# Kernel optimization log

Hardware: AMD Instinct MI355X
Metric: run time of the kernel (lower is better)

Reference implementation:

```python
import jax, jax.numpy as jnp
import numpy as np

WS = 4      # window_size (RSUT5 default)
SHIFT = 2   # window_size // 2
NH = 8      # num_heads
DIM = 256
H0 = W0 = T0 = 32
B0 = 1


def _ln(x, g, b, eps=1e-5):
    m = x.mean(-1, keepdims=True)
    v = ((x - m) ** 2).mean(-1, keepdims=True)
    return (x - m) / jnp.sqrt(v + eps) * g + b


def _rel_index(ws):
    c = np.stack(np.meshgrid(np.arange(ws), np.arange(ws), np.arange(ws), indexing='ij')).reshape(3, -1)
    r = (c[:, :, None] - c[:, None, :]).transpose(1, 2, 0) + (ws - 1)
    return jnp.asarray((r[..., 0] * (2 * ws - 1) + r[..., 1]) * (2 * ws - 1) + r[..., 2])


def _partition(x, ws):
    B, H, W, T, C = x.shape
    x = x.reshape(B, H // ws, ws, W // ws, ws, T // ws, ws, C)
    return x.transpose(0, 1, 3, 5, 2, 4, 6, 7).reshape(-1, ws ** 3, C)


def _reverse(w, ws, B, H, W, T):
    C = w.shape[-1]
    x = w.reshape(B, H // ws, W // ws, T // ws, ws, ws, ws, C)
    return x.transpose(0, 1, 4, 2, 5, 3, 6, 7).reshape(B, H, W, T, C)


def _attn_mask(H, W, T, ws, ss):
    # static (numpy) replica of Block.createmask; H,W,T divisible by ws here
    img = np.zeros((H, W, T), np.float32)
    sls = (slice(0, -ws), slice(-ws, -ss), slice(-ss, None))
    cnt = 0
    for h in sls:
        for w in sls:
            for t in sls:
                img[h, w, t] = cnt
                cnt += 1
    mw = img.reshape(H // ws, ws, W // ws, ws, T // ws, ws).transpose(0, 2, 4, 1, 3, 5).reshape(-1, ws ** 3)
    d = mw[:, None, :] - mw[:, :, None]
    return jnp.asarray(np.where(d != 0, -100.0, 0.0).astype(np.float32))


def _swin(x, H, W, T, shift, mask, n1g, n1b, qkvw, qkvb, rpb, projw, projb, n2g, n2b, fc1w, fc1b, fc2w, fc2b):
    B, L, C = x.shape
    N = WS ** 3
    hd = C // NH
    shortcut = x
    x = _ln(x, n1g, n1b).reshape(B, H, W, T, C)
    if shift:
        x = jnp.roll(x, (-shift, -shift, -shift), axis=(1, 2, 3))
    xw = _partition(x, WS)                                        # [B*nW, N, C]
    qkv = (xw @ qkvw.T + qkvb).reshape(-1, N, 3, NH, hd).transpose(2, 0, 3, 1, 4)
    q, k, v = qkv[0], qkv[1], qkv[2]                              # [B*nW, NH, N, hd]
    attn = jnp.einsum('bhnd,bhmd->bhnm', q * (hd ** -0.5), k)
    attn = attn + rpb[_rel_index(WS)].transpose(2, 0, 1)[None]    # relative position bias
    if mask is not None:
        nW = mask.shape[0]
        attn = (attn.reshape(B, nW, NH, N, N) + mask[None, :, None]).reshape(-1, NH, N, N)
    attn = jax.nn.softmax(attn, axis=-1)
    out = jnp.einsum('bhnm,bhmd->bhnd', attn, v).transpose(0, 2, 1, 3).reshape(-1, N, C)
    out = out @ projw.T + projb
    x = _reverse(out, WS, B, H, W, T)
    if shift:
        x = jnp.roll(x, (shift, shift, shift), axis=(1, 2, 3))
    x = shortcut + x.reshape(B, L, C)
    h = _ln(x, n2g, n2b)
    h = jax.nn.gelu(h @ fc1w.T + fc1b, approximate=False) @ fc2w.T + fc2b
    return x + h


def setup_inputs() -> dict:
    key = jax.random.key(0)
    ks = iter(jax.random.split(key, 16))
    def rn(shape, s=0.02):
        return jax.random.normal(next(ks), shape, jnp.float32) * s
    d = {'x': jax.random.normal(next(ks), (B0, H0 * W0 * T0, DIM), jnp.float32),
         'H': H0, 'W': W0, 'T': T0,
         'norm_g': jnp.ones((DIM,), jnp.float32), 'norm_b': jnp.zeros((DIM,), jnp.float32)}
    for p in ('w', 's'):
        d[p + 'n1g'] = jnp.ones((DIM,), jnp.float32); d[p + 'n1b'] = jnp.zeros((DIM,), jnp.float32)
        d[p + 'qkvw'] = rn((3 * DIM, DIM)); d[p + 'qkvb'] = jnp.zeros((3 * DIM,), jnp.float32)
        d[p + 'rpb'] = rn(((2 * WS - 1) ** 3, NH))
        d[p + 'projw'] = rn((DIM, DIM)); d[p + 'projb'] = jnp.zeros((DIM,), jnp.float32)
        d[p + 'n2g'] = jnp.ones((DIM,), jnp.float32); d[p + 'n2b'] = jnp.zeros((DIM,), jnp.float32)
        d[p + 'fc1w'] = rn((4 * DIM, DIM)); d[p + 'fc1b'] = jnp.zeros((4 * DIM,), jnp.float32)
        d[p + 'fc2w'] = rn((DIM, 4 * DIM)); d[p + 'fc2b'] = jnp.zeros((DIM,), jnp.float32)
    return d


def reference(x, H, W, T, norm_g, norm_b,
              wn1g, wn1b, wqkvw, wqkvb, wrpb, wprojw, wprojb, wn2g, wn2b, wfc1w, wfc1b, wfc2w, wfc2b,
              sn1g, sn1b, sqkvw, sqkvb, srpb, sprojw, sprojb, sn2g, sn2b, sfc1w, sfc1b, sfc2w, sfc2b):
    mask = _attn_mask(H, W, T, WS, SHIFT)
    x = _swin(x, H, W, T, 0, None, wn1g, wn1b, wqkvw, wqkvb, wrpb, wprojw, wprojb, wn2g, wn2b, wfc1w, wfc1b, wfc2w, wfc2b)
    x = _swin(x, H, W, T, SHIFT, mask, sn1g, sn1b, sqkvw, sqkvb, srpb, sprojw, sprojb, sn2g, sn2b, sfc1w, sfc1b, sfc2w, sfc2b)
    B, L, C = x.shape
    # Block.norm + toConv: [B, L, C] -> [B, C, H, W, T]
    return _ln(x, norm_g, norm_b).reshape(B, H, W, T, C).transpose(0, 4, 1, 2, 3)
```

## Files before the change

kernel.cpp:

```cpp
#include <hip/hip_runtime.h>

typedef unsigned short u16;
typedef unsigned int   u32;
typedef __bf16 bfx8 __attribute__((ext_vector_type(8)));
typedef float  fx4  __attribute__((ext_vector_type(4)));

__device__ __forceinline__ u16 f2b(float f) {
    union { float f; u32 i; } v; v.f = f;
    u32 r = (v.i + 0x7fffu + ((v.i >> 16) & 1u)) >> 16;
    return (u16)r;
}
__device__ __forceinline__ u32 pk(float a, float b) {
    return (u32)f2b(a) | ((u32)f2b(b) << 16);
}

__device__ __forceinline__ void gl2lds16(const u16* g, u16* l) {
    __builtin_amdgcn_global_load_lds(
        (const __attribute__((address_space(1))) u32*)(const void*)g,
        (__attribute__((address_space(3))) u32*)(void*)l, 16, 0, 0);
}

__device__ __forceinline__ int map_token(int r, int shift) {
    int win = r >> 6, n = r & 63;
    int wh = win >> 6, ww = (win >> 3) & 7, wt = win & 7;
    int h = wh * 4 + (n >> 4);
    int w = ww * 4 + ((n >> 2) & 3);
    int t = wt * 4 + (n & 3);
    h = (h + shift) & 31; w = (w + shift) & 31; t = (t + shift) & 31;
    return (h << 10) | (w << 5) | t;
}

__device__ __forceinline__ float gelu_fast(float v) {
    float t = v * v;
    float u = v * __builtin_fmaf(t, 0.044715f, 1.0f);
    float e = __expf(-1.5957691216057308f * u);
    return v * __builtin_amdgcn_rcpf(1.0f + e);
}

struct CvtArgs { const float* src[8]; int cum[9]; };
__global__ __launch_bounds__(256) void cvt_kernel(CvtArgs a, u16* __restrict__ dst) {
    int g = (blockIdx.x * 256 + threadIdx.x) * 4;
    int t = 0;
    #pragma unroll
    for (int i = 1; i < 8; i++) t += (g >= a.cum[i]);
    int local = g - a.cum[t];
    float4 f = *(const float4*)(a.src[t] + local);
    uint2 o; o.x = pk(f.x, f.y); o.y = pk(f.z, f.w);
    *(uint2*)(dst + g) = o;
}

template<int GATHER, int F32OUT>
__global__ __launch_bounds__(256) void ln_kernel(const float* __restrict__ resid,
                                                 const float* __restrict__ g, const float* __restrict__ b,
                                                 void* __restrict__ outp, int shift) {
    int lane = threadIdx.x & 63;
    int row  = blockIdx.x * 4 + (threadIdx.x >> 6);
    int src  = GATHER ? map_token(row, shift) : row;
    float4 x = ((const float4*)(resid + src * 256))[lane];
    float s1 = x.x + x.y + x.z + x.w;
    float s2 = x.x * x.x + x.y * x.y + x.z * x.z + x.w * x.w;
    #pragma unroll
    for (int off = 1; off < 64; off <<= 1) { s1 += __shfl_xor(s1, off); s2 += __shfl_xor(s2, off); }
    float mean = s1 * (1.0f / 256.0f);
    float var  = s2 * (1.0f / 256.0f) - mean * mean;
    float rstd = rsqrtf(var + 1e-5f);
    int c = lane * 4;
    float4 gv = *(const float4*)(g + c);
    float4 bv = *(const float4*)(b + c);
    float y0 = (x.x - mean) * rstd * gv.x + bv.x;
    float y1 = (x.y - mean) * rstd * gv.y + bv.y;
    float y2 = (x.z - mean) * rstd * gv.z + bv.z;
    float y3 = (x.w - mean) * rstd * gv.w + bv.w;
    if (F32OUT) {
        float4 o; o.x = y0; o.y = y1; o.z = y2; o.w = y3;
        *(float4*)((float*)outp + row * 256 + c) = o;
    } else {
        uint2 o; o.x = pk(y0, y1); o.y = pk(y2, y3);
        *(uint2*)((u16*)outp + row * 256 + c) = o;
    }
}

template<int EPI>
__global__ __launch_bounds__(256) void gemm2(const u16* __restrict__ A, const u16* __restrict__ W,
                                             const float* __restrict__ bias,
                                             u16* __restrict__ outb, float* __restrict__ resid,
                                             int Nout, int K, int shift,
                                             const float* __restrict__ rsrc) {
    __shared__ u16 As[3][4096];
    __shared__ u16 Bs[3][4096];
    int lane = threadIdx.x & 63, w = threadIdx.x >> 6;
    int wm = w >> 1, wn = w & 1;
    int m0 = blockIdx.x * 128, n0 = blockIdx.y * 128;
    int lr = lane & 15, q = lane >> 4;
    int sw = q ^ ((lr >> 1) & 3);

    int rowS  = w * 16 + (lane >> 2);
    int kg    = (lane & 3) ^ ((rowS >> 1) & 3);
    int slot0 = (w * 64 + lane) * 8;
    int slot1 = slot0 + 2048;
    const u16* gA0 = A + (size_t)(m0 + rowS) * K + kg * 8;
    const u16* gA1 = A + (size_t)(m0 + rowS + 64) * K + kg * 8;
    const u16* gB0 = W + (size_t)(n0 + rowS) * K + kg * 8;
    const u16* gB1 = W + (size_t)(n0 + rowS + 64) * K + kg * 8;

    int oA[4], oB[4];
    #pragma unroll
    for (int t = 0; t < 4; t++) {
        oA[t] = ((wm * 64 + t * 16 + lr) * 4 + sw) * 8;
        oB[t] = ((wn * 64 + t * 16 + lr) * 4 + sw) * 8;
    }

    fx4 acc[4][4] = {};

    auto stage = [&](int kt, int b) {
        gl2lds16(gA0 + kt, &As[b][slot0]);
        gl2lds16(gA1 + kt, &As[b][slot1]);
        gl2lds16(gB0 + kt, &Bs[b][slot0]);
        gl2lds16(gB1 + kt, &Bs[b][slot1]);
    };

    int nk = K >> 5;
    stage(0, 0);
    if (nk > 1) stage(32, 1);
    int b0 = 0, b1 = 1, b2 = 2;
    for (int ki = 0; ki < nk; ki++) {
        if (ki + 1 < nk) asm volatile("s_waitcnt vmcnt(4)" ::: "memory");
        else             asm volatile("s_waitcnt vmcnt(0)" ::: "memory");
        __builtin_amdgcn_s_barrier();
        __builtin_amdgcn_sched_barrier(0);
        if (ki + 2 < nk) stage((ki + 2) << 5, b2);
        bfx8 af[4], bfr[4];
        #pragma unroll
        for (int t = 0; t < 4; t++) {
            af[t]  = *(const bfx8*)(&As[b0][oA[t]]);
            bfr[t] = *(const bfx8*)(&Bs[b0][oB[t]]);
        }
        #pragma unroll
        for (int i = 0; i < 4; i++)
            #pragma unroll
            for (int j = 0; j < 4; j++)
                acc[i][j] = __builtin_amdgcn_mfma_f32_16x16x32_bf16(af[i], bfr[j], acc[i][j], 0, 0, 0);
        int tmp = b0; b0 = b1; b1 = b2; b2 = tmp;
    }

    float bv[4];
    #pragma unroll
    for (int j = 0; j < 4; j++) bv[j] = bias[n0 + wn * 64 + j * 16 + lr];
    #pragma unroll
    for (int i = 0; i < 4; i++) {
        #pragma unroll
        for (int r = 0; r < 4; r++) {
            int gr = m0 + wm * 64 + i * 16 + q * 4 + r;
            int orow = (EPI == 3) ? map_token(gr, shift) : gr;
            #pragma unroll
            for (int j = 0; j < 4; j++) {
                int gc = n0 + wn * 64 + j * 16 + lr;
                float v = acc[i][j][r] + bv[j];
                if (EPI == 0) {
                    outb[(size_t)gr * Nout + gc] = f2b(v);
                } else if (EPI == 1) {
                    outb[(size_t)gr * Nout + gc] = f2b(gelu_fast(v));
                } else {
                    resid[orow * 256 + gc] = rsrc[orow * 256 + gc] + v;
                }
            }
        }
    }
}

__global__ __launch_bounds__(128) void attn_mfma(const u16* __restrict__ qkv, const float* __restrict__ rpb,
                                                 u16* __restrict__ outb, int masked) {
    __shared__ u16  Pl[2][64][72];
    __shared__ u16  VT[2][32][72];
    __shared__ float rbS[2][344];
    int w = threadIdx.x >> 6;
    int lane = threadIdx.x & 63;
    int id = blockIdx.x * 2 + w;
    int win = id >> 3, head = id & 7;
    int lr = lane & 15, q = lane >> 4;

    const u16* base = qkv + (size_t)win * 64 * 768 + head * 32;

    bfx8 qf[4], kf[4];
    #pragma unroll
    for (int t = 0; t < 4; t++) {
        const u16* rq = base + (lr + 16 * t) * 768 + q * 8;
        qf[t] = *(const bfx8*)(rq);
        kf[t] = *(const bfx8*)(rq + 256);
    }
    {
        const u16* rv = base + lane * 768 + 512;
        #pragma unroll
        for (int c = 0; c < 32; c += 8) {
            bfx8 vv = *(const bfx8*)(rv + c);
            #pragma unroll
            for (int j = 0; j < 8; j++) VT[w][c + j][lane] = ((const u16*)&vv)[j];
        }
    }
    for (int i = lane; i < 343; i += 64) rbS[w][i] = rpb[i * 8 + head];

    fx4 sT[4][4] = {};
    #pragma unroll
    for (int jt = 0; jt < 4; jt++)
        #pragma unroll
        for (int it = 0; it < 4; it++)
            sT[jt][it] = __builtin_amdgcn_mfma_f32_16x16x32_bf16(kf[jt], qf[it], sT[jt][it], 0, 0, 0);

    int wh = win >> 6, ww = (win >> 3) & 7, wt = win & 7;
    const float scale = 0.17677669529663687f;

    #pragma unroll
    for (int it = 0; it < 4; it++) {
        int i = lr + 16 * it;
        int ih = i >> 4, iw = (i >> 2) & 3, iT = i & 3;
        int labn = 0;
        if (masked) {
            int lh = (wh == 7) ? (1 + (ih >> 1)) : 0;
            int lw = (ww == 7) ? (1 + (iw >> 1)) : 0;
            int lt = (wt == 7) ? (1 + (iT >> 1)) : 0;
            labn = lh * 9 + lw * 3 + lt;
        }
        float sv[4][4];
        float mx = -1e30f;
        #pragma unroll
        for (int jt = 0; jt < 4; jt++)
            #pragma unroll
            for (int r = 0; r < 4; r++) {
                int j = q * 4 + r + 16 * jt;
                int jh = j >> 4, jw = (j >> 2) & 3, jT = j & 3;
                float s = sT[jt][it][r] * scale +
                          rbS[w][((ih - jh + 3) * 7 + (iw - jw + 3)) * 7 + (iT - jT + 3)];
                if (masked) {
                    int lh = (wh == 7) ? (1 + (jh >> 1)) : 0;
                    int lw = (ww == 7) ? (1 + (jw >> 1)) : 0;
                    int lt = (wt == 7) ? (1 + (jT >> 1)) : 0;
                    if (lh * 9 + lw * 3 + lt != labn) s -= 100.0f;
                }
                sv[jt][r] = s;
                mx = fmaxf(mx, s);
            }
        mx = fmaxf(mx, __shfl_xor(mx, 16));
        mx = fmaxf(mx, __shfl_xor(mx, 32));
        float sum = 0.f;
        #pragma unroll
        for (int jt = 0; jt < 4; jt++)
            #pragma unroll
            for (int r = 0; r < 4; r++) { sv[jt][r] = __expf(sv[jt][r] - mx); sum += sv[jt][r]; }
        sum += __shfl_xor(sum, 16);
        sum += __shfl_xor(sum, 32);
        float inv = 1.0f / sum;
        #pragma unroll
        for (int jt = 0; jt < 4; jt++) {
            uint2 pw;
            pw.x = pk(sv[jt][0] * inv, sv[jt][1] * inv);
            pw.y = pk(sv[jt][2] * inv, sv[jt][3] * inv);
            *(uint2*)&Pl[w][i][q * 4 + 16 * jt] = pw;
        }
    }

    fx4 o[4][2] = {};
    #pragma unroll
    for (int kk = 0; kk < 2; kk++) {
        bfx8 pf[4], vf[2];
        #pragma unroll
        for (int it = 0; it < 4; it++) pf[it] = *(const bfx8*)&Pl[w][lr + 16 * it][q * 8 + 32 * kk];
        #pragma unroll
        for (int dt = 0; dt < 2; dt++) vf[dt] = *(const bfx8*)&VT[w][lr + 16 * dt][q * 8 + 32 * kk];
        #pragma unroll
        for (int it = 0; it < 4; it++)
            #pragma unroll
            for (int dt = 0; dt < 2; dt++)
                o[it][dt] = __builtin_amdgcn_mfma_f32_16x16x32_bf16(pf[it], vf[dt], o[it][dt], 0, 0, 0);
    }

    u16* ob = outb + (size_t)win * 64 * 256 + head * 32;
    #pragma unroll
    for (int it = 0; it < 4; it++)
        #pragma unroll
        for (int r = 0; r < 4; r++) {
            int i = 16 * it + q * 4 + r;
            #pragma unroll
            for (int dt = 0; dt < 2; dt++)
                ob[i * 256 + 16 * dt + lr] = f2b(o[it][dt][r]);
        }
}

__global__ __launch_bounds__(256) void ln_tr(const float* __restrict__ in,
                                             const float* __restrict__ g, const float* __restrict__ b,
                                             float* __restrict__ out) {
    __shared__ float tile[256 * 33];
    int tid = threadIdx.x;
    int r   = tid >> 3;
    int cg  = (tid & 7) * 32;
    int row = blockIdx.x * 32 + r;
    const float* src = in + (size_t)row * 256 + cg;

    float v[32];
    float s1 = 0.f, s2 = 0.f;
    #pragma unroll
    for (int j = 0; j < 8; j++) {
        float4 f = *(const float4*)(src + 4 * j);
        v[4*j] = f.x; v[4*j+1] = f.y; v[4*j+2] = f.z; v[4*j+3] = f.w;
        s1 += f.x + f.y + f.z + f.w;
        s2 += f.x*f.x + f.y*f.y + f.z*f.z + f.w*f.w;
    }
    #pragma unroll
    for (int off = 1; off < 8; off <<= 1) { s1 += __shfl_xor(s1, off); s2 += __shfl_xor(s2, off); }
    float mean = s1 * (1.0f / 256.0f);
    float rstd = rsqrtf(s2 * (1.0f / 256.0f) - mean * mean + 1e-5f);

    #pragma unroll
    for (int j = 0; j < 8; j++) {
        float4 gv = *(const float4*)(g + cg + 4 * j);
        float4 bv = *(const float4*)(b + cg + 4 * j);
        int c0 = cg + 4 * j;
        int slot = (r + (c0 >> 2)) & 31;
        tile[(c0 + 0) * 33 + slot] = (v[4*j]   - mean) * rstd * gv.x + bv.x;
        tile[(c0 + 1) * 33 + slot] = (v[4*j+1] - mean) * rstd * gv.y + bv.y;
        tile[(c0 + 2) * 33 + slot] = (v[4*j+2] - mean) * rstd * gv.z + bv.z;
        tile[(c0 + 3) * 33 + slot] = (v[4*j+3] - mean) * rstd * gv.w + bv.w;
    }
    __syncthreads();

    int c = tid;
    int csh = (c >> 2) & 31;
    const float* base = &tile[c * 33];
    float o[32];
    #pragma unroll
    for (int r2 = 0; r2 < 32; r2++) o[r2] = base[(r2 + csh) & 31];

    float* dst = out + (size_t)c * 32768 + blockIdx.x * 32;
    #pragma unroll
    for (int j = 0; j < 8; j++) {
        float4 f; f.x = o[4*j]; f.y = o[4*j+1]; f.z = o[4*j+2]; f.w = o[4*j+3];
        *(float4*)(dst + 4 * j) = f;
    }
}

extern "C" void kernel_launch(void* const* d_in, const int* in_sizes, int n_in,
                              void* d_out, int out_size, void* d_ws, size_t ws_size,
                              hipStream_t stream) {
    const float* x      = (const float*)d_in[0];
    const float* norm_g = (const float*)d_in[4];
    const float* norm_b = (const float*)d_in[5];

    char* wsb = (char*)d_ws;
    float* resid = (float*)wsb;
    u16*   xn    = (u16*)(wsb + (size_t)32 * 1024 * 1024);
    u16*   big   = (u16*)(wsb + (size_t)48 * 1024 * 1024);
    u16*   attnb = (u16*)(wsb + (size_t)96 * 1024 * 1024);
    u16*   wb    = (u16*)(wsb + (size_t)112 * 1024 * 1024);

    CvtArgs ca;
    static const int offs[9] = {0, 196608, 262144, 524288, 786432, 983040, 1048576, 1310720, 1572864};
    for (int i = 0; i < 9; i++) ca.cum[i] = offs[i];
    ca.src[0] = (const float*)d_in[6 + 2];
    ca.src[1] = (const float*)d_in[6 + 5];
    ca.src[2] = (const float*)d_in[6 + 9];
    ca.src[3] = (const float*)d_in[6 + 11];
    ca.src[4] = (const float*)d_in[19 + 2];
    ca.src[5] = (const float*)d_in[19 + 5];
    ca.src[6] = (const float*)d_in[19 + 9];
    ca.src[7] = (const float*)d_in[19 + 11];
    cvt_kernel<<<1536, 256, 0, stream>>>(ca, wb);

    for (int blk = 0; blk < 2; blk++) {
        void* const* P = d_in + 6 + blk * 13;
        const float* n1g  = (const float*)P[0];
        const float* n1b  = (const float*)P[1];
        const float* qkvb = (const float*)P[3];
        const float* rpb  = (const float*)P[4];
        const float* pjb  = (const float*)P[6];
        const float* n2g  = (const float*)P[7];
        const float* n2b  = (const float*)P[8];
        const float* f1b  = (const float*)P[10];
        const float* f2b_ = (const float*)P[12];
        const u16* qkvw = wb + offs[0] + blk * 786432;
        const u16* pjw  = wb + offs[1] + blk * 786432;
        const u16* f1w  = wb + offs[2] + blk * 786432;
        const u16* f2w  = wb + offs[3] + blk * 786432;
        int shift = blk ? 2 : 0;

        const float* ln1src = blk ? resid : x;
        const float* projadd = blk ? resid : x;

        ln_kernel<1, 0><<<8192, 256, 0, stream>>>(ln1src, n1g, n1b, xn, shift);
        gemm2<0><<<dim3(256, 6), 256, 0, stream>>>(xn, qkvw, qkvb, big, nullptr, 768, 256, 0, nullptr);
        attn_mfma<<<2048, 128, 0, stream>>>(big, rpb, attnb, blk);
        gemm2<3><<<dim3(256, 2), 256, 0, stream>>>(attnb, pjw, pjb, nullptr, resid, 256, 256, shift, projadd);
        ln_kernel<0, 0><<<8192, 256, 0, stream>>>(resid, n2g, n2b, xn, 0);
        gemm2<1><<<dim3(256, 8), 256, 0, stream>>>(xn, f1w, f1b, big, nullptr, 1024, 256, 0, nullptr);
        gemm2<2><<<dim3(256, 2), 256, 0, stream>>>(big, f2w, f2b_, nullptr, resid, 256, 1024, 0, resid);
    }

    ln_tr<<<1024, 256, 0, stream>>>(resid, norm_g, norm_b, (float*)d_out);
}
```

Baseline: 467.4 us.

## Add 8-wave 256x128 GEMM with interleaved LDS prefetch for QKV and FC1

```diff
diff --git a/kernel.cpp b/kernel.cpp
--- a/kernel.cpp
+++ b/kernel.cpp
@@ -81,6 +81,149 @@
 }
 
 template<int EPI>
+__global__ __launch_bounds__(512) void gemm8(const u16* __restrict__ A, const u16* __restrict__ W,
+                                             const float* __restrict__ bias,
+                                             u16* __restrict__ outb, int Nout, int K) {
+    __shared__ u16 AS[2][16384];
+    __shared__ u16 BS[2][8192];
+    int tid = threadIdx.x;
+    int lane = tid & 63, w = tid >> 6;
+    int wm = w >> 1, wn = w & 1;
+    int m0 = blockIdx.x * 256, n0 = blockIdx.y * 128;
+    int lr = lane & 15, q = lane >> 4;
+
+    int srow = tid >> 3;
+    int scol = ((tid & 7) ^ (srow & 7)) * 8;
+    const size_t kA = (size_t)64 * K;
+    const u16* gA = A + (size_t)(m0 + srow) * K + scol;
+    const u16* gB = W + (size_t)(n0 + srow) * K + scol;
+
+    int oA[2][4], oB[2][4];
+    #pragma unroll
+    for (int ks = 0; ks < 2; ks++)
+        #pragma unroll
+        for (int t = 0; t < 4; t++) {
+            int ra = wm * 64 + t * 16 + lr;
+            int rb = wn * 64 + t * 16 + lr;
+            int g  = ((ks << 2) + q) ^ (lr & 7);
+            oA[ks][t] = ra * 64 + g * 8;
+            oB[ks][t] = rb * 64 + g * 8;
+        }
+
+    fx4 acc[4][4] = {};
+    int nt = K >> 6;
+
+    {
+        u16* dA = &AS[0][0] + tid * 8;
+        u16* dB = &BS[0][0] + tid * 8;
+        gl2lds16(gA,          dA);
+        gl2lds16(gA + kA,     dA + 4096);
+        gl2lds16(gA + 2 * kA, dA + 8192);
+        gl2lds16(gA + 3 * kA, dA + 12288);
+        gl2lds16(gB,          dB);
+        gl2lds16(gB + kA,     dB + 4096);
+    }
+    asm volatile("s_waitcnt vmcnt(0)" ::: "memory");
+    __builtin_amdgcn_s_barrier();
+
+    for (int t = 0; t < nt; t++) {
+        const u16* as = &AS[t & 1][0];
+        const u16* bs = &BS[t & 1][0];
+        u16* da = &AS[(t + 1) & 1][0] + tid * 8;
+        u16* db = &BS[(t + 1) & 1][0] + tid * 8;
+        const u16* ga = gA + (size_t)(t + 1) * 64;
+        const u16* gb = gB + (size_t)(t + 1) * 64;
+        int st = (t + 1 < nt);
+        bfx8 a[4], b01[2], b23[2];
+
+        a[0]   = *(const bfx8*)(as + oA[0][0]);
+        a[1]   = *(const bfx8*)(as + oA[0][1]);
+        a[2]   = *(const bfx8*)(as + oA[0][2]);
+        a[3]   = *(const bfx8*)(as + oA[0][3]);
+        b01[0] = *(const bfx8*)(bs + oB[0][0]);
+        b01[1] = *(const bfx8*)(bs + oB[0][1]);
+        if (st) { gl2lds16(ga, da); gl2lds16(ga + kA, da + 4096); }
+        __builtin_amdgcn_s_barrier();
+        asm volatile("s_waitcnt lgkmcnt(0)" ::: "memory");
+        __builtin_amdgcn_sched_barrier(0);
+        __builtin_amdgcn_s_setprio(1);
+        #pragma unroll
+        for (int i = 0; i < 4; i++) {
+            acc[i][0] = __builtin_amdgcn_mfma_f32_16x16x32_bf16(a[i], b01[0], acc[i][0], 0, 0, 0);
+            acc[i][1] = __builtin_amdgcn_mfma_f32_16x16x32_bf16(a[i], b01[1], acc[i][1], 0, 0, 0);
+        }
+        __builtin_amdgcn_s_setprio(0);
+        __builtin_amdgcn_s_barrier();
+
+        b23[0] = *(const bfx8*)(bs + oB[0][2]);
+        b23[1] = *(const bfx8*)(bs + oB[0][3]);
+        if (st) { gl2lds16(ga + 2 * kA, da + 8192); gl2lds16(ga + 3 * kA, da + 12288); }
+        __builtin_amdgcn_s_barrier();
+        asm volatile("s_waitcnt lgkmcnt(0)" ::: "memory");
+        __builtin_amdgcn_sched_barrier(0);
+        __builtin_amdgcn_s_setprio(1);
+        #pragma unroll
+        for (int i = 0; i < 4; i++) {
+            acc[i][2] = __builtin_amdgcn_mfma_f32_16x16x32_bf16(a[i], b23[0], acc[i][2], 0, 0, 0);
+            acc[i][3] = __builtin_amdgcn_mfma_f32_16x16x32_bf16(a[i], b23[1], acc[i][3], 0, 0, 0);
+        }
+        __builtin_amdgcn_s_setprio(0);
+        __builtin_amdgcn_s_barrier();
+
+        a[0]   = *(const bfx8*)(as + oA[1][0]);
+        a[1]   = *(const bfx8*)(as + oA[1][1]);
+        a[2]   = *(const bfx8*)(as + oA[1][2]);
+        a[3]   = *(const bfx8*)(as + oA[1][3]);
+        b01[0] = *(const bfx8*)(bs + oB[1][0]);
+        b01[1] = *(const bfx8*)(bs + oB[1][1]);
+        if (st) { gl2lds16(gb, db); gl2lds16(gb + kA, db + 4096); }
+        __builtin_amdgcn_s_barrier();
+        asm volatile("s_waitcnt lgkmcnt(0)" ::: "memory");
+        __builtin_amdgcn_sched_barrier(0);
+        __builtin_amdgcn_s_setprio(1);
+        #pragma unroll
+        for (int i = 0; i < 4; i++) {
+            acc[i][0] = __builtin_amdgcn_mfma_f32_16x16x32_bf16(a[i], b01[0], acc[i][0], 0, 0, 0);
+            acc[i][1] = __builtin_amdgcn_mfma_f32_16x16x32_bf16(a[i], b01[1], acc[i][1], 0, 0, 0);
+        }
+        __builtin_amdgcn_s_setprio(0);
+        __builtin_amdgcn_s_barrier();
+
+        b23[0] = *(const bfx8*)(bs + oB[1][2]);
+        b23[1] = *(const bfx8*)(bs + oB[1][3]);
+        __builtin_amdgcn_s_barrier();
+        asm volatile("s_waitcnt lgkmcnt(0)" ::: "memory");
+        __builtin_amdgcn_sched_barrier(0);
+        __builtin_amdgcn_s_setprio(1);
+        #pragma unroll
+        for (int i = 0; i < 4; i++) {
+            acc[i][2] = __builtin_amdgcn_mfma_f32_16x16x32_bf16(a[i], b23[0], acc[i][2], 0, 0, 0);
+            acc[i][3] = __builtin_amdgcn_mfma_f32_16x16x32_bf16(a[i], b23[1], acc[i][3], 0, 0, 0);
+        }
+        __builtin_amdgcn_s_setprio(0);
+        asm volatile("s_waitcnt vmcnt(0)" ::: "memory");
+        __builtin_amdgcn_s_barrier();
+    }
+
+    float bv[4];
+    #pragma unroll
+    for (int j = 0; j < 4; j++) bv[j] = bias[n0 + wn * 64 + j * 16 + lr];
+    #pragma unroll
+    for (int i = 0; i < 4; i++) {
+        #pragma unroll
+        for (int r = 0; r < 4; r++) {
+            int gr = m0 + wm * 64 + i * 16 + q * 4 + r;
+            #pragma unroll
+            for (int j = 0; j < 4; j++) {
+                int gc = n0 + wn * 64 + j * 16 + lr;
+                float v = acc[i][j][r] + bv[j];
+                outb[(size_t)gr * Nout + gc] = f2b(EPI == 1 ? gelu_fast(v) : v);
+            }
+        }
+    }
+}
+
+template<int EPI>
 __global__ __launch_bounds__(256) void gemm2(const u16* __restrict__ A, const u16* __restrict__ W,
                                              const float* __restrict__ bias,
                                              u16* __restrict__ outb, float* __restrict__ resid,
@@ -385,11 +528,11 @@
         const float* projadd = blk ? resid : x;
 
         ln_kernel<1, 0><<<8192, 256, 0, stream>>>(ln1src, n1g, n1b, xn, shift);
-        gemm2<0><<<dim3(256, 6), 256, 0, stream>>>(xn, qkvw, qkvb, big, nullptr, 768, 256, 0, nullptr);
+        gemm8<0><<<dim3(128, 6), 512, 0, stream>>>(xn, qkvw, qkvb, big, 768, 256);
         attn_mfma<<<2048, 128, 0, stream>>>(big, rpb, attnb, blk);
         gemm2<3><<<dim3(256, 2), 256, 0, stream>>>(attnb, pjw, pjb, nullptr, resid, 256, 256, shift, projadd);
         ln_kernel<0, 0><<<8192, 256, 0, stream>>>(resid, n2g, n2b, xn, 0);
-        gemm2<1><<<dim3(256, 8), 256, 0, stream>>>(xn, f1w, f1b, big, nullptr, 1024, 256, 0, nullptr);
+        gemm8<1><<<dim3(128, 8), 512, 0, stream>>>(xn, f1w, f1b, big, 1024, 256);
         gemm2<2><<<dim3(256, 2), 256, 0, stream>>>(big, f2w, f2b_, nullptr, resid, 256, 1024, 0, resid);
     }
 
```

Measured after the change: 489.5 us. 4.7% more time.

## Fuse residual-add GEMMs with following LayerNorm into single full-row kernel

Applied to the files above, without the earlier changes.

```diff
diff --git a/kernel.cpp b/kernel.cpp
--- a/kernel.cpp
+++ b/kernel.cpp
@@ -28,6 +28,13 @@
     int t = wt * 4 + (n & 3);
     h = (h + shift) & 31; w = (w + shift) & 31; t = (t + shift) & 31;
     return (h << 10) | (w << 5) | t;
+}
+__device__ __forceinline__ int map_inv(int tok, int shift) {
+    int h = (((tok >> 10) & 31) - shift) & 31;
+    int w = (((tok >> 5) & 31) - shift) & 31;
+    int t = ((tok & 31) - shift) & 31;
+    return (((h >> 2) * 64 + (w >> 2) * 8 + (t >> 2)) << 6) |
+           ((h & 3) * 16 + (w & 3) * 4 + (t & 3));
 }
 
 __device__ __forceinline__ float gelu_fast(float v) {
@@ -168,6 +175,144 @@
     }
 }
 
+template<int MODE>
+__global__ __launch_bounds__(256) void gemmln(const u16* __restrict__ A, const u16* __restrict__ W,
+                                              const float* __restrict__ bias,
+                                              const float* __restrict__ rsrc, float* __restrict__ resid,
+                                              u16* __restrict__ xn,
+                                              const float* __restrict__ lg, const float* __restrict__ lb,
+                                              int K, int shift) {
+    __shared__ u16 As[3][2048];
+    __shared__ u16 Bs[3][8192];
+    __shared__ float red[2][4][64];
+    int tid = threadIdx.x;
+    int lane = tid & 63, wn = tid >> 6;
+    int m0 = blockIdx.x * 64;
+    int lr = lane & 15, q = lane >> 4;
+    int sw = q ^ ((lr >> 1) & 3);
+
+    int rowS = tid >> 2;
+    int kg   = (tid & 3) ^ ((rowS >> 1) & 3);
+    const size_t sK = (size_t)64 * K;
+    const u16* gA = A + (size_t)(m0 + rowS) * K + kg * 8;
+    const u16* gB = W + (size_t)rowS * K + kg * 8;
+
+    int oA[4], oB[4];
+    #pragma unroll
+    for (int t = 0; t < 4; t++) {
+        oA[t] = ((t * 16 + lr) * 4 + sw) * 8;
+        oB[t] = (((wn * 64 + t * 16 + lr)) * 4 + sw) * 8;
+    }
+
+    fx4 acc[4][4] = {};
+
+    auto stage = [&](int kt, int b) {
+        gl2lds16(gA + kt, &As[b][tid * 8]);
+        #pragma unroll
+        for (int s = 0; s < 4; s++)
+            gl2lds16(gB + s * sK + kt, &Bs[b][s * 2048 + tid * 8]);
+    };
+
+    int nk = K >> 5;
+    stage(0, 0);
+    if (nk > 1) stage(32, 1);
+    int b0 = 0, b1 = 1, b2 = 2;
+    for (int ki = 0; ki < nk; ki++) {
+        if (ki + 1 < nk) asm volatile("s_waitcnt vmcnt(5)" ::: "memory");
+        else             asm volatile("s_waitcnt vmcnt(0)" ::: "memory");
+        __builtin_amdgcn_s_barrier();
+        __builtin_amdgcn_sched_barrier(0);
+        if (ki + 2 < nk) stage((ki + 2) << 5, b2);
+        bfx8 af[4], bfr[4];
+        #pragma unroll
+        for (int t = 0; t < 4; t++) {
+            af[t]  = *(const bfx8*)(&As[b0][oA[t]]);
+            bfr[t] = *(const bfx8*)(&Bs[b0][oB[t]]);
+        }
+        #pragma unroll
+        for (int i = 0; i < 4; i++)
+            #pragma unroll
+            for (int j = 0; j < 4; j++)
+                acc[i][j] = __builtin_amdgcn_mfma_f32_16x16x32_bf16(af[i], bfr[j], acc[i][j], 0, 0, 0);
+        int tmp = b0; b0 = b1; b1 = b2; b2 = tmp;
+    }
+
+    float bv[4], gv[4], bbv[4];
+    #pragma unroll
+    for (int j = 0; j < 4; j++) {
+        int col = wn * 64 + j * 16 + lr;
+        bv[j] = bias[col]; gv[j] = lg[col]; bbv[j] = lb[col];
+    }
+
+    int orow[4][4];
+    #pragma unroll
+    for (int i = 0; i < 4; i++)
+        #pragma unroll
+        for (int r = 0; r < 4; r++) {
+            int gr = m0 + i * 16 + q * 4 + r;
+            orow[i][r] = (MODE == 0) ? map_token(gr, shift) : gr;
+        }
+
+    float rs[4][4][4];
+    float s1[4][4], s2[4][4];
+    #pragma unroll
+    for (int i = 0; i < 4; i++)
+        #pragma unroll
+        for (int r = 0; r < 4; r++) {
+            float a1 = 0.f, a2 = 0.f;
+            #pragma unroll
+            for (int j = 0; j < 4; j++) {
+                int col = wn * 64 + j * 16 + lr;
+                float rv = rsrc[orow[i][r] * 256 + col];
+                rs[i][r][j] = rv;
+                float v = rv + acc[i][j][r] + bv[j];
+                a1 += v; a2 += v * v;
+            }
+            s1[i][r] = a1; s2[i][r] = a2;
+        }
+    #pragma unroll
+    for (int i = 0; i < 4; i++)
+        #pragma unroll
+        for (int r = 0; r < 4; r++) {
+            #pragma unroll
+            for (int off = 1; off < 16; off <<= 1) {
+                s1[i][r] += __shfl_xor(s1[i][r], off);
+                s2[i][r] += __shfl_xor(s2[i][r], off);
+            }
+        }
+    if (lr == 0) {
+        #pragma unroll
+        for (int i = 0; i < 4; i++)
+            #pragma unroll
+            for (int r = 0; r < 4; r++) {
+                int rl = i * 16 + q * 4 + r;
+                red[0][wn][rl] = s1[i][r];
+                red[1][wn][rl] = s2[i][r];
+            }
+    }
+    __syncthreads();
+
+    #pragma unroll
+    for (int i = 0; i < 4; i++)
+        #pragma unroll
+        for (int r = 0; r < 4; r++) {
+            int rl = i * 16 + q * 4 + r;
+            float S1 = red[0][0][rl] + red[0][1][rl] + red[0][2][rl] + red[0][3][rl];
+            float S2 = red[1][0][rl] + red[1][1][rl] + red[1][2][rl] + red[1][3][rl];
+            float mean = S1 * (1.0f / 256.0f);
+            float rstd = rsqrtf(S2 * (1.0f / 256.0f) - mean * mean + 1e-5f);
+            int gr = m0 + rl;
+            int xrow = (MODE == 0) ? orow[i][r] : map_inv(gr, shift);
+            #pragma unroll
+            for (int j = 0; j < 4; j++) {
+                int col = wn * 64 + j * 16 + lr;
+                float v = rs[i][r][j] + acc[i][j][r] + bv[j];
+                resid[orow[i][r] * 256 + col] = v;
+                xn[xrow * 256 + col] = f2b((v - mean) * rstd * gv[j] + bbv[j]);
+            }
+        }
+}
+
 __global__ __launch_bounds__(128) void attn_mfma(const u16* __restrict__ qkv, const float* __restrict__ rpb,
                                                  u16* __restrict__ outb, int masked) {
     __shared__ u16  Pl[2][64][72];
@@ -364,34 +509,32 @@
     ca.src[7] = (const float*)d_in[19 + 11];
     cvt_kernel<<<1536, 256, 0, stream>>>(ca, wb);
 
-    for (int blk = 0; blk < 2; blk++) {
-        void* const* P = d_in + 6 + blk * 13;
-        const float* n1g  = (const float*)P[0];
-        const float* n1b  = (const float*)P[1];
-        const float* qkvb = (const float*)P[3];
-        const float* rpb  = (const float*)P[4];
-        const float* pjb  = (const float*)P[6];
-        const float* n2g  = (const float*)P[7];
-        const float* n2b  = (const float*)P[8];
-        const float* f1b  = (const float*)P[10];
-        const float* f2b_ = (const float*)P[12];
-        const u16* qkvw = wb + offs[0] + blk * 786432;
-        const u16* pjw  = wb + offs[1] + blk * 786432;
-        const u16* f1w  = wb + offs[2] + blk * 786432;
-        const u16* f2w  = wb + offs[3] + blk * 786432;
-        int shift = blk ? 2 : 0;
-
-        const float* ln1src = blk ? resid : x;
-        const float* projadd = blk ? resid : x;
-
-        ln_kernel<1, 0><<<8192, 256, 0, stream>>>(ln1src, n1g, n1b, xn, shift);
-        gemm2<0><<<dim3(256, 6), 256, 0, stream>>>(xn, qkvw, qkvb, big, nullptr, 768, 256, 0, nullptr);
-        attn_mfma<<<2048, 128, 0, stream>>>(big, rpb, attnb, blk);
-        gemm2<3><<<dim3(256, 2), 256, 0, stream>>>(attnb, pjw, pjb, nullptr, resid, 256, 256, shift, projadd);
-        ln_kernel<0, 0><<<8192, 256, 0, stream>>>(resid, n2g, n2b, xn, 0);
-        gemm2<1><<<dim3(256, 8), 256, 0, stream>>>(xn, f1w, f1b, big, nullptr, 1024, 256, 0, nullptr);
-        gemm2<2><<<dim3(256, 2), 256, 0, stream>>>(big, f2w, f2b_, nullptr, resid, 256, 1024, 0, resid);
-    }
+    void* const* P0 = d_in + 6;
+    void* const* P1 = d_in + 19;
+    const u16* qkvw0 = wb + offs[0];
+    const u16* pjw0  = wb + offs[1];
+    const u16* f1w0  = wb + offs[2];
+    const u16* f2w0  = wb + offs[3];
+    const u16* qkvw1 = wb + offs[0] + 786432;
+    const u16* pjw1  = wb + offs[1] + 786432;
+    const u16* f1w1  = wb + offs[2] + 786432;
+    const u16* f2w1  = wb + offs[3] + 786432;
+
+    ln_kernel<1, 0><<<8192, 256, 0, stream>>>(x, (const float*)P0[0], (const float*)P0[1], xn, 0);
+    gemm2<0><<<dim3(256, 6), 256, 0, stream>>>(xn, qkvw0, (const float*)P0[3], big, nullptr, 768, 256, 0, nullptr);
+    attn_mfma<<<2048, 128, 0, stream>>>(big, (const float*)P0[4], attnb, 0);
+    gemmln<0><<<512, 256, 0, stream>>>(attnb, pjw0, (const float*)P0[6], x, resid, xn,
+                                       (const float*)P0[7], (const float*)P0[8], 256, 0);
+    gemm2<1><<<dim3(256, 8), 256, 0, stream>>>(xn, f1w0, (const float*)P0[10], big, nullptr, 1024, 256, 0, nullptr);
+    gemmln<1><<<512, 256, 0, stream>>>(big, f2w0, (const float*)P0[12], resid, resid, xn,
+                                       (const float*)P1[0], (const float*)P1[1], 1024, 2);
+
+    gemm2<0><<<dim3(256, 6), 256, 0, stream>>>(xn, qkvw1, (const float*)P1[3], big, nullptr, 768, 256, 0, nullptr);
+    attn_mfma<<<2048, 128, 0, stream>>>(big, (const float*)P1[4], attnb, 1);
+    gemmln<0><<<512, 256, 0, stream>>>(attnb, pjw1, (const float*)P1[6], resid, resid, xn,
+                                       (const float*)P1[7], (const float*)P1[8], 256, 2);
+    gemm2<1><<<dim3(256, 8), 256, 0, stream>>>(xn, f1w1, (const float*)P1[10], big, nullptr, 1024, 256, 0, nullptr);
+    gemm2<2><<<dim3(256, 2), 256, 0, stream>>>(big, f2w1, (const float*)P1[12], nullptr, resid, 256, 1024, 0, resid);
 
     ln_tr<<<1024, 256, 0, stream>>>(resid, norm_g, norm_b, (float*)d_out);
 }
```

Result: slower. 481.3 us (+3.0%).
